# Optimization experiments

Hardware: AMD Instinct MI355X
Metric: run time of the kernel (lower is better)

Reference implementation:

```python
import jax, jax.numpy as jnp
import numpy as np

B, L, D, H, T = 64, 512, 768, 384, 9  # batch, seq_len, hidden, hidden//2, num_tags


def setup_inputs() -> dict:
    key = jax.random.key(0)
    ks = jax.random.split(key, 8)
    return {
        "encoder_out": jax.random.normal(ks[0], (B, L, D), jnp.float32),
        "ner_labels": jax.random.randint(ks[1], (B, L), 0, T),
        "mask": jnp.ones((B, L), jnp.bool_),
        "W1": jax.random.normal(ks[2], (D, H), jnp.float32) / np.sqrt(D).astype(np.float32),
        "b1": jnp.zeros((H,), jnp.float32),
        "W2": jax.random.normal(ks[3], (H, T), jnp.float32) / np.sqrt(H).astype(np.float32),
        "b2": jnp.zeros((T,), jnp.float32),
        "start_trans": jax.random.uniform(ks[4], (T,), jnp.float32, -0.1, 0.1),
        "end_trans": jax.random.uniform(ks[5], (T,), jnp.float32, -0.1, 0.1),
        "trans": jax.random.uniform(ks[6], (T, T), jnp.float32, -0.1, 0.1),
    }


def _crf_nll(emissions, tags, mask, start_trans, end_trans, trans):
    """-mean log-likelihood, matching pytorch-crf forward (reduction='mean')."""
    maskf = mask.astype(emissions.dtype)
    # ---- numerator: score of the gold tag path ----
    emit = jnp.take_along_axis(emissions, tags[..., None], axis=-1)[..., 0]  # [B,L]
    emit_score = jnp.sum(emit * maskf, axis=1)
    tr = trans[tags[:, :-1], tags[:, 1:]]  # [B,L-1]
    tr_score = jnp.sum(tr * maskf[:, 1:], axis=1)
    last_idx = jnp.sum(mask.astype(jnp.int32), axis=1) - 1
    last_tags = jnp.take_along_axis(tags, last_idx[:, None], axis=1)[:, 0]
    numer = start_trans[tags[:, 0]] + emit_score + tr_score + end_trans[last_tags]
    # ---- denominator: forward algorithm (log partition) via scan ----
    alpha0 = start_trans[None, :] + emissions[:, 0]          # [B,T]
    em_rest = jnp.swapaxes(emissions[:, 1:], 0, 1)           # [L-1,B,T]
    mk_rest = jnp.swapaxes(maskf[:, 1:], 0, 1)               # [L-1,B]

    def step(alpha, xs):
        e_t, m_t = xs
        nxt = jax.nn.logsumexp(alpha[:, :, None] + trans[None, :, :] + e_t[:, None, :], axis=1)
        return jnp.where(m_t[:, None] > 0, nxt, alpha), None

    alpha, _ = jax.lax.scan(step, alpha0, (em_rest, mk_rest))
    denom = jax.nn.logsumexp(alpha + end_trans[None, :], axis=1)
    return -jnp.mean(numer - denom)


def reference(encoder_out, ner_labels, mask, W1, b1, W2, b2, start_trans, end_trans, trans):
    # proj: Linear -> GELU (exact erf, torch default) -> Dropout (identity in eval)
    h = jax.nn.gelu(encoder_out @ W1 + b1, approximate=False)
    emissions = h @ W2 + b2  # [B,L,T]
    return _crf_nll(emissions, ner_labels, mask, start_trans, end_trans, trans)
```

## Files before the change

kernel.cpp:

```cpp
#include <hip/hip_runtime.h>
#include <hip/hip_bf16.h>
#include <math.h>

#define B_ 64
#define L_ 512
#define D_ 768
#define H_ 384
#define T_ 9
#define M_ (B_ * L_)

typedef __attribute__((ext_vector_type(8))) short short8;
typedef __attribute__((ext_vector_type(4))) float f32x4;

__device__ __forceinline__ unsigned short f2bf(float f) {
    unsigned u = __float_as_uint(f);
    u += 0x7FFFu + ((u >> 16) & 1u);
    return (unsigned short)(u >> 16);
}

__device__ __forceinline__ unsigned pkbf2(float a, float b) {
    __hip_bfloat162 h = __float22bfloat162_rn(float2{a, b});
    return *(unsigned*)&h;
}

__device__ __forceinline__ float gelu_fast(float x) {
    float z2 = 1.5957691216f * x + 0.0713548162726f * x * x * x;
    return x / (1.f + __expf(-z2));
}

__device__ __forceinline__ float wredf(float v) {
#pragma unroll
    for (int m = 32; m >= 1; m >>= 1) v += __shfl_xor(v, m, 64);
    return v;
}

__device__ __forceinline__ short8 pack8(f32x4 a, f32x4 b) {
    int4 v = {(int)pkbf2(a[0], a[1]), (int)pkbf2(a[2], a[3]),
              (int)pkbf2(b[0], b[1]), (int)pkbf2(b[2], b[3])};
    return *(short8*)&v;
}

__device__ __forceinline__ void stage16(const float* g, void* l) {
    __builtin_amdgcn_global_load_lds(
        (const __attribute__((address_space(1))) void*)g,
        (__attribute__((address_space(3))) void*)l, 16, 0, 0);
}

__global__ __launch_bounds__(256) void prep_kernel(
    const float* __restrict__ W1, const float* __restrict__ W2,
    unsigned short* __restrict__ W1F, unsigned short* __restrict__ W2F,
    float* __restrict__ out)
{
    if (blockIdx.x == 0 && threadIdx.x == 0) out[0] = 0.f;
    const int g    = blockIdx.x * 4 + (threadIdx.x >> 6);
    const int lane = threadIdx.x & 63;
    const int lm   = lane & 15;
    const int q    = lane >> 4;
    if (g < 576) {
        const int nt = g / 24;
        const int kc = g - nt * 24;
        const int n  = nt * 16 + lm;
        short8 v;
#pragma unroll
        for (int j = 0; j < 8; ++j)
            v[j] = (short)f2bf(W1[(size_t)(kc * 32 + q * 8 + j) * H_ + n]);
        *(short8*)(W1F + ((size_t)g * 64 + lane) * 8) = v;
    } else if (g < 588) {
        const int kk = g - 576;
        short8 v;
#pragma unroll
        for (int j = 0; j < 8; ++j) {
            int k = kk * 32 + q * 8 + j;
            v[j] = (lm < 9) ? (short)f2bf(W2[(size_t)k * T_ + lm]) : (short)0;
        }
        *(short8*)(W2F + ((size_t)kk * 64 + lane) * 8) = v;
    }
}

__global__ __launch_bounds__(256, 5) void emis_mfma_kernel(
    const float* __restrict__ X,
    const unsigned short* __restrict__ W1F,
    const float* __restrict__ b1,
    const unsigned short* __restrict__ W2F,
    const float* __restrict__ b2,
    float* __restrict__ em0,
    float* __restrict__ em1)
{
    __shared__ __align__(16) unsigned short Hs[32 * 200];
    float* AsF = (float*)Hs;

    const int t    = threadIdx.x;
    const int lane = t & 63;
    const int w    = t >> 6;
    const int lm   = lane & 15;
    const int q    = lane >> 4;
    const int half = blockIdx.x >> 10;
    const int rb   = blockIdx.x & 1023;
    const int row0 = rb * 32;

    const int sr = t >> 3;
    const int sc = (t & 7) ^ (sr & 7);
    const float* sp = X + (size_t)(row0 + sr) * D_ + sc * 4;
    char* l0 = (char*)Hs + w * 1024;
    char* l1 = l0 + 4096;

    const int ntg0 = half * 12 + w * 3;

    const int e7  = lm & 7;
    const int co0 = (((q * 2 + 0) ^ e7) << 2);
    const int co1 = (((q * 2 + 1) ^ e7) << 2);

    f32x4 acc[2][3];
#pragma unroll
    for (int mt = 0; mt < 2; ++mt)
#pragma unroll
        for (int i = 0; i < 3; ++i) acc[mt][i] = (f32x4)0.f;

    stage16(sp, l0);
    short8 bb[3];
#pragma unroll
    for (int i = 0; i < 3; ++i)
        bb[i] = *(const short8*)(W1F + (((size_t)(ntg0 + i) * 24 + 0) * 64 + lane) * 8);
    asm volatile("s_waitcnt vmcnt(0)" ::: "memory");
    __builtin_amdgcn_s_barrier();

#pragma unroll
    for (int kc = 0; kc < 24; ++kc) {
        const int s = kc & 1;
        if (kc < 23) stage16(sp + (kc + 1) * 32, s ? l0 : l1);
        short8 bbn[3];
        if (kc < 23) {
#pragma unroll
            for (int i = 0; i < 3; ++i)
                bbn[i] = *(const short8*)(W1F +
                    (((size_t)(ntg0 + i) * 24 + kc + 1) * 64 + lane) * 8);
        }
        const float* fb = AsF + s * 1024;
        short8 af[2];
#pragma unroll
        for (int mt = 0; mt < 2; ++mt) {
            const float* rp = fb + (mt * 16 + lm) * 32;
            f32x4 a0 = *(const f32x4*)(rp + co0);
            f32x4 a1 = *(const f32x4*)(rp + co1);
            af[mt] = pack8(a0, a1);
        }
#pragma unroll
        for (int mt = 0; mt < 2; ++mt)
#pragma unroll
            for (int i = 0; i < 3; ++i)
                acc[mt][i] = __builtin_amdgcn_mfma_f32_16x16x32_bf16(
                    af[mt], bb[i], acc[mt][i], 0, 0, 0);
        if (kc < 23) {
#pragma unroll
            for (int i = 0; i < 3; ++i) bb[i] = bbn[i];
            asm volatile("s_waitcnt vmcnt(0)" ::: "memory");
            __builtin_amdgcn_s_barrier();
        }
    }
    __syncthreads();

#pragma unroll
    for (int i = 0; i < 3; ++i) {
        const int lc = w * 48 + i * 16 + lm;
        const float b1v = b1[half * 192 + lc];
#pragma unroll
        for (int mt = 0; mt < 2; ++mt)
#pragma unroll
            for (int r = 0; r < 4; ++r) {
                float h = gelu_fast(acc[mt][i][r] + b1v);
                Hs[(mt * 16 + q * 4 + r) * 200 + lc] = f2bf(h);
            }
    }
    __syncthreads();

    if (w < 2) {
        f32x4 e = (f32x4)0.f;
#pragma unroll
        for (int kk = 0; kk < 6; ++kk) {
            short8 ah = *(const short8*)&Hs[(w * 16 + lm) * 200 + kk * 32 + (q << 3)];
            short8 bw = *(const short8*)(W2F + ((size_t)((half * 6 + kk) * 64 + lane)) * 8);
            e = __builtin_amdgcn_mfma_f32_16x16x32_bf16(ah, bw, e, 0, 0, 0);
        }
        if (lm < 9) {
            float* emo = half ? em1 : em0;
            const float badd = half ? 0.f : b2[lm];
#pragma unroll
            for (int r = 0; r < 4; ++r)
                emo[(size_t)(row0 + w * 16 + q * 4 + r) * T_ + lm] = e[r] + badd;
        }
    }
}

__global__ __launch_bounds__(640) void crf_kernel(
    const float* __restrict__ em0,
    const float* __restrict__ em1,
    const int* __restrict__ labels,
    const unsigned char* __restrict__ maskb,
    const float* __restrict__ st,
    const float* __restrict__ et,
    const float* __restrict__ tr,
    float* __restrict__ out)
{
    const int b = blockIdx.x;
    const int t = threadIdx.x;

    __shared__ float es[64 * 73];
    __shared__ float Msa[64 * 81];
    __shared__ float Msb[32 * 81];
    __shared__ float trs[81];
    __shared__ float red_num;
    __shared__ unsigned char msh[L_];
    __shared__ int lbs[L_];

    const int mstride =
        (maskb[0] != 0 && maskb[1] == 0 && maskb[2] == 0 && maskb[3] == 0) ? 4 : 1;

    const float* e0 = em0 + (size_t)b * L_ * T_;
    const float* e1 = em1 + (size_t)b * L_ * T_;
    for (int i = t; i < L_ * T_; i += 640) {
        int tt = i / T_, j = i - tt * T_;
        es[(tt >> 3) * 73 + (tt & 7) * 9 + j] = e0[i] + e1[i];
    }
    if (t < 81) trs[t] = tr[t];
    for (int i = t; i < L_; i += 640) {
        msh[i] = maskb[((size_t)b * L_ + i) * (size_t)mstride];
        lbs[i] = labels[b * L_ + i];
    }
    __syncthreads();

    if (t < 576) {
        const int c  = t / 9;
        const int i0 = t - c * 9;
        float trr[81];
#pragma unroll
        for (int i = 0; i < 81; ++i) trr[i] = trs[i];
        float V[9];
#pragma unroll
        for (int j = 0; j < 9; ++j) V[j] = (j == i0) ? 0.f : -1e30f;

        const int sbeg = (c == 0) ? 1 : 0;
        for (int s = sbeg; s < 8; ++s) {
            int tt = c * 8 + s;
            if (msh[tt]) {
                const float* ep = &es[c * 73 + s * 9];
                float nv[9];
#pragma unroll
                for (int j = 0; j < 9; ++j) {
                    float a[9];
#pragma unroll
                    for (int k = 0; k < 9; ++k) a[k] = V[k] + trr[k * 9 + j];
                    float mx = a[0];
#pragma unroll
                    for (int k = 1; k < 9; ++k) mx = fmaxf(mx, a[k]);
                    float sum = 0.f;
#pragma unroll
                    for (int k = 0; k < 9; ++k) sum += __expf(a[k] - mx);
                    nv[j] = ep[j] + mx + __logf(sum);
                }
#pragma unroll
                for (int j = 0; j < 9; ++j) V[j] = nv[j];
            }
        }
#pragma unroll
        for (int j = 0; j < 9; ++j) Msa[c * 81 + i0 * 9 + j] = V[j];
    } else {
        const int lane = t - 576;
        float emit_s = 0.f, tr_sc = 0.f, mcnt = 0.f;
        for (int tt = lane; tt < L_; tt += 64) {
            if (msh[tt]) {
                mcnt += 1.f;
                int tag = lbs[tt];
                emit_s += es[(tt >> 3) * 73 + (tt & 7) * 9 + tag];
                if (tt >= 1) tr_sc += trs[lbs[tt - 1] * 9 + tag];
            }
        }
        emit_s = wredf(emit_s);
        tr_sc  = wredf(tr_sc);
        mcnt   = wredf(mcnt);
        if (lane == 0) {
            int last = (int)mcnt - 1;
            red_num = st[lbs[0]] + emit_s + tr_sc + et[lbs[last]];
        }
    }
    __syncthreads();

    float* src = Msa;
    float* dst = Msb;
    for (int n = 32; n >= 1; n >>= 1) {
        for (int idx = t; idx < n * 81; idx += 640) {
            int p = idx / 81;
            int r = idx - p * 81;
            int i = r / 9, j = r - i * 9;
            const float* A  = src + (2 * p) * 81 + i * 9;
            const float* Bm = src + (2 * p + 1) * 81 + j;
            float v[9];
#pragma unroll
            for (int k = 0; k < 9; ++k) v[k] = A[k] + Bm[k * 9];
            float mx = v[0];
#pragma unroll
            for (int k = 1; k < 9; ++k) mx = fmaxf(mx, v[k]);
            float sum = 0.f;
#pragma unroll
            for (int k = 0; k < 9; ++k) sum += __expf(v[k] - mx);
            dst[p * 81 + r] = mx + __logf(sum);
        }
        __syncthreads();
        float* tmp = src; src = dst; dst = tmp;
    }

    if (t < 64) {
        float v = -3.0e38f;
        if (t < 9) {
            float a[9];
#pragma unroll
            for (int i = 0; i < 9; ++i) a[i] = st[i] + es[i] + src[i * 9 + t];
            float mx = a[0];
#pragma unroll
            for (int i = 1; i < 9; ++i) mx = fmaxf(mx, a[i]);
            float sum = 0.f;
#pragma unroll
            for (int i = 0; i < 9; ++i) sum += __expf(a[i] - mx);
            v = mx + __logf(sum) + et[t];
        }
        float mx = v;
#pragma unroll
        for (int m = 32; m >= 1; m >>= 1) mx = fmaxf(mx, __shfl_xor(mx, m, 64));
        float sm = __expf(v - mx);
        sm = wredf(sm);
        if (t == 0) {
            float denom = mx + __logf(sm);
            atomicAdd(out, (denom - red_num) * (1.0f / (float)B_));
        }
    }
}

extern "C" void kernel_launch(void* const* d_in, const int* in_sizes, int n_in,
                              void* d_out, int out_size, void* d_ws, size_t ws_size,
                              hipStream_t stream) {
    const float*         enc    = (const float*)d_in[0];
    const int*           labels = (const int*)d_in[1];
    const unsigned char* mask   = (const unsigned char*)d_in[2];
    const float*         W1     = (const float*)d_in[3];
    const float*         b1     = (const float*)d_in[4];
    const float*         W2     = (const float*)d_in[5];
    const float*         b2     = (const float*)d_in[6];
    const float*         st     = (const float*)d_in[7];
    const float*         et     = (const float*)d_in[8];
    const float*         tr     = (const float*)d_in[9];

    float* em0          = (float*)d_ws;
    float* em1          = em0 + (size_t)M_ * T_;
    unsigned short* W1F = (unsigned short*)(em1 + (size_t)M_ * T_);
    unsigned short* W2F = W1F + (size_t)576 * 64 * 8;

    prep_kernel<<<147, 256, 0, stream>>>(W1, W2, W1F, W2F, (float*)d_out);
    emis_mfma_kernel<<<2048, 256, 0, stream>>>(enc, W1F, b1, W2F, b2, em0, em1);
    crf_kernel<<<B_, 640, 0, stream>>>(em0, em1, labels, mask, st, et, tr, (float*)d_out);
}
```

Baseline: 242.1 us.

## Double M-tile per block and deepen A/B prefetch to four-stage pipeline

Each emission block now processes 64 rows instead of 32, halving the grid and doubling reuse of each W1 fragment across four M-subtiles. The LDS staging for X becomes a four-buffer ring, and W1 fragments use a three-deep register ring. The wait is now a partial vmcnt before each barrier instead of a full drain, so global loads stay in flight across iterations. This is meant to hide load latency and cut W1 traffic, at the cost of more registers and LDS (occupancy hint lowered to 4) and fewer blocks.

After: 237.6 us. No clear change (-1.8%).

```diff
diff --git a/kernel.cpp b/kernel.cpp
--- a/kernel.cpp
+++ b/kernel.cpp
@@ -45,6 +45,8 @@
         (const __attribute__((address_space(1))) void*)g,
         (__attribute__((address_space(3))) void*)l, 16, 0, 0);
 }
+
+#define SBAR() __builtin_amdgcn_sched_barrier(0)
 
 __global__ __launch_bounds__(256) void prep_kernel(
     const float* __restrict__ W1, const float* __restrict__ W2,
@@ -77,7 +79,7 @@
     }
 }
 
-__global__ __launch_bounds__(256, 5) void emis_mfma_kernel(
+__global__ __launch_bounds__(256, 4) void emis_mfma_kernel(
     const float* __restrict__ X,
     const unsigned short* __restrict__ W1F,
     const float* __restrict__ b1,
@@ -86,23 +88,22 @@
     float* __restrict__ em0,
     float* __restrict__ em1)
 {
-    __shared__ __align__(16) unsigned short Hs[32 * 200];
-    float* AsF = (float*)Hs;
+    __shared__ __align__(16) char smem[32768];
+    unsigned short* Hs = (unsigned short*)smem;
 
     const int t    = threadIdx.x;
     const int lane = t & 63;
     const int w    = t >> 6;
     const int lm   = lane & 15;
     const int q    = lane >> 4;
-    const int half = blockIdx.x >> 10;
-    const int rb   = blockIdx.x & 1023;
-    const int row0 = rb * 32;
-
-    const int sr = t >> 3;
-    const int sc = (t & 7) ^ (sr & 7);
-    const float* sp = X + (size_t)(row0 + sr) * D_ + sc * 4;
-    char* l0 = (char*)Hs + w * 1024;
-    char* l1 = l0 + 4096;
+    const int half = blockIdx.x >> 9;
+    const int rb   = blockIdx.x & 511;
+    const int row0 = rb * 64;
+
+    const int r0 = t >> 3;
+    const int c  = (t & 7) ^ (r0 & 7);
+    const float* sp  = X + (size_t)(row0 + r0) * D_ + c * 4;
+    const float* sp1 = sp + (size_t)32 * D_;
 
     const int ntg0 = half * 12 + w * 3;
 
@@ -110,53 +111,67 @@
     const int co0 = (((q * 2 + 0) ^ e7) << 2);
     const int co1 = (((q * 2 + 1) ^ e7) << 2);
 
-    f32x4 acc[2][3];
-#pragma unroll
-    for (int mt = 0; mt < 2; ++mt)
+    f32x4 acc[4][3];
+#pragma unroll
+    for (int mt = 0; mt < 4; ++mt)
 #pragma unroll
         for (int i = 0; i < 3; ++i) acc[mt][i] = (f32x4)0.f;
 
-    stage16(sp, l0);
-    short8 bb[3];
+    short8 bb[3][3];
+
+    stage16(sp,       smem + 0     + w * 1024);
+    stage16(sp1,      smem + 4096  + w * 1024);
 #pragma unroll
     for (int i = 0; i < 3; ++i)
-        bb[i] = *(const short8*)(W1F + (((size_t)(ntg0 + i) * 24 + 0) * 64 + lane) * 8);
-    asm volatile("s_waitcnt vmcnt(0)" ::: "memory");
-    __builtin_amdgcn_s_barrier();
+        bb[0][i] = *(const short8*)(W1F + (((size_t)(ntg0 + i) * 24 + 0) * 64 + lane) * 8);
+    SBAR();
+    stage16(sp + 32,  smem + 8192  + w * 1024);
+    stage16(sp1 + 32, smem + 12288 + w * 1024);
+#pragma unroll
+    for (int i = 0; i < 3; ++i)
+        bb[1][i] = *(const short8*)(W1F + (((size_t)(ntg0 + i) * 24 + 1) * 64 + lane) * 8);
+    SBAR();
+    stage16(sp + 64,  smem + 16384 + w * 1024);
+    stage16(sp1 + 64, smem + 20480 + w * 1024);
+    SBAR();
 
 #pragma unroll
     for (int kc = 0; kc < 24; ++kc) {
-        const int s = kc & 1;
-        if (kc < 23) stage16(sp + (kc + 1) * 32, s ? l0 : l1);
-        short8 bbn[3];
-        if (kc < 23) {
+        const int cb = kc & 3;
+        asm volatile("s_waitcnt vmcnt(7)\n\ts_barrier" ::: "memory");
+        SBAR();
+        {
+            const int kb = (kc + 2 <= 23) ? kc + 2 : 23;
 #pragma unroll
             for (int i = 0; i < 3; ++i)
-                bbn[i] = *(const short8*)(W1F +
-                    (((size_t)(ntg0 + i) * 24 + kc + 1) * 64 + lane) * 8);
-        }
-        const float* fb = AsF + s * 1024;
-        short8 af[2];
-#pragma unroll
-        for (int mt = 0; mt < 2; ++mt) {
+                bb[(kc + 2) % 3][i] = *(const short8*)(W1F +
+                    (((size_t)(ntg0 + i) * 24 + kb) * 64 + lane) * 8);
+        }
+        SBAR();
+        {
+            const int ks = (kc + 3 <= 23) ? kc + 3 : 23;
+            const int sb = (kc + 3) & 3;
+            stage16(sp  + ks * 32, smem + sb * 8192        + w * 1024);
+            stage16(sp1 + ks * 32, smem + sb * 8192 + 4096 + w * 1024);
+        }
+        SBAR();
+        const float* fb = (const float*)(smem + cb * 8192);
+        short8 af[4];
+#pragma unroll
+        for (int mt = 0; mt < 4; ++mt) {
             const float* rp = fb + (mt * 16 + lm) * 32;
             f32x4 a0 = *(const f32x4*)(rp + co0);
             f32x4 a1 = *(const f32x4*)(rp + co1);
             af[mt] = pack8(a0, a1);
         }
 #pragma unroll
-        for (int mt = 0; mt < 2; ++mt)
+        for (int mt = 0; mt < 4; ++mt)
 #pragma unroll
             for (int i = 0; i < 3; ++i)
                 acc[mt][i] = __builtin_amdgcn_mfma_f32_16x16x32_bf16(
-                    af[mt], bb[i], acc[mt][i], 0, 0, 0);
-        if (kc < 23) {
-#pragma unroll
-            for (int i = 0; i < 3; ++i) bb[i] = bbn[i];
-            asm volatile("s_waitcnt vmcnt(0)" ::: "memory");
-            __builtin_amdgcn_s_barrier();
-        }
-    }
+                    af[mt], bb[kc % 3][i], acc[mt][i], 0, 0, 0);
+    }
+    asm volatile("s_waitcnt vmcnt(0)" ::: "memory");
     __syncthreads();
 
 #pragma unroll
@@ -164,7 +179,7 @@
         const int lc = w * 48 + i * 16 + lm;
         const float b1v = b1[half * 192 + lc];
 #pragma unroll
-        for (int mt = 0; mt < 2; ++mt)
+        for (int mt = 0; mt < 4; ++mt)
 #pragma unroll
             for (int r = 0; r < 4; ++r) {
                 float h = gelu_fast(acc[mt][i][r] + b1v);
@@ -173,21 +188,19 @@
     }
     __syncthreads();
 
-    if (w < 2) {
-        f32x4 e = (f32x4)0.f;
-#pragma unroll
-        for (int kk = 0; kk < 6; ++kk) {
-            short8 ah = *(const short8*)&Hs[(w * 16 + lm) * 200 + kk * 32 + (q << 3)];
-            short8 bw = *(const short8*)(W2F + ((size_t)((half * 6 + kk) * 64 + lane)) * 8);
-            e = __builtin_amdgcn_mfma_f32_16x16x32_bf16(ah, bw, e, 0, 0, 0);
-        }
-        if (lm < 9) {
-            float* emo = half ? em1 : em0;
-            const float badd = half ? 0.f : b2[lm];
-#pragma unroll
-            for (int r = 0; r < 4; ++r)
-                emo[(size_t)(row0 + w * 16 + q * 4 + r) * T_ + lm] = e[r] + badd;
-        }
+    f32x4 e = (f32x4)0.f;
+#pragma unroll
+    for (int kk = 0; kk < 6; ++kk) {
+        short8 ah = *(const short8*)&Hs[(w * 16 + lm) * 200 + kk * 32 + (q << 3)];
+        short8 bw = *(const short8*)(W2F + ((size_t)((half * 6 + kk) * 64 + lane)) * 8);
+        e = __builtin_amdgcn_mfma_f32_16x16x32_bf16(ah, bw, e, 0, 0, 0);
+    }
+    if (lm < 9) {
+        float* emo = half ? em1 : em0;
+        const float badd = half ? 0.f : b2[lm];
+#pragma unroll
+        for (int r = 0; r < 4; ++r)
+            emo[(size_t)(row0 + w * 16 + q * 4 + r) * T_ + lm] = e[r] + badd;
     }
 }
 
@@ -354,6 +367,6 @@
     unsigned short* W2F = W1F + (size_t)576 * 64 * 8;
 
     prep_kernel<<<147, 256, 0, stream>>>(W1, W2, W1F, W2F, (float*)d_out);
-    emis_mfma_kernel<<<2048, 256, 0, stream>>>(enc, W1F, b1, W2F, b2, em0, em1);
+    emis_mfma_kernel<<<1024, 256, 0, stream>>>(enc, W1F, b1, W2F, b2, em0, em1);
     crf_kernel<<<B_, 640, 0, stream>>>(em0, em1, labels, mask, st, et, tr, (float*)d_out);
 }
```
